# Performance work log

Measured on AMD Instinct MI355X. Metric: run time of the kernel, lower is better.

The kernel has to match this reference:

```python
import jax, jax.numpy as jnp
import numpy as np

HIDDEN = 1024
NUM_HEADS = 16
HEAD_SIZE = HIDDEN // NUM_HEADS


def setup_inputs() -> dict:
    key = jax.random.key(0)
    ks = jax.random.split(key, 5)
    B, S = 2, 2048
    x = jax.random.normal(ks[0], (B, S, HIDDEN), dtype=jnp.float32)
    # nn.Linear(hidden, 3*hidden): weight stored (in, out) for x @ W
    scale_qkv = 1.0 / np.sqrt(HIDDEN)
    w_qkv = jax.random.uniform(ks[1], (HIDDEN, 3 * HIDDEN), minval=-scale_qkv, maxval=scale_qkv, dtype=jnp.float32)
    b_qkv = jax.random.uniform(ks[2], (3 * HIDDEN,), minval=-scale_qkv, maxval=scale_qkv, dtype=jnp.float32)
    w_o = jax.random.uniform(ks[3], (HIDDEN, HIDDEN), minval=-scale_qkv, maxval=scale_qkv, dtype=jnp.float32)
    b_o = jax.random.uniform(ks[4], (HIDDEN,), minval=-scale_qkv, maxval=scale_qkv, dtype=jnp.float32)
    return {"x": x, "w_qkv": w_qkv, "b_qkv": b_qkv, "w_o": w_o, "b_o": b_o}


def reference(x, w_qkv, b_qkv, w_o, b_o):
    B, S, H = x.shape
    qkv = x @ w_qkv + b_qkv  # (B, S, 3H)
    q, k, v = jnp.split(qkv, 3, axis=-1)
    # (B, S, H) -> (B, nheads, S, head_size)
    def heads(t):
        return t.reshape(B, S, NUM_HEADS, HEAD_SIZE).transpose(0, 2, 1, 3)
    q, k, v = heads(q), heads(k), heads(v)
    scores = jnp.einsum('bhqd,bhkd->bhqk', q, k) / np.sqrt(HEAD_SIZE).astype(np.float32)
    causal = jnp.tril(jnp.ones((S, S), dtype=bool))  # k <= q
    scores = jnp.where(causal, scores, -jnp.inf)
    probs = jax.nn.softmax(scores, axis=-1)
    out = jnp.einsum('bhqk,bhkd->bqhd', probs, v).reshape(B, S, H)
    return out @ w_o + b_o
```

## Files before the change

kernel.cpp:

```cpp
#include <hip/hip_runtime.h>
#include <stdint.h>


typedef __bf16 bf16;
typedef __attribute__((ext_vector_type(8))) __bf16 bf16x8;
typedef __attribute__((ext_vector_type(4))) __bf16 bf16x4;
typedef __attribute__((ext_vector_type(4))) float floatx4;
typedef __attribute__((ext_vector_type(16))) float floatx16;

#define SCL 0.18033688011112042f

__device__ __forceinline__ floatx4 mfma_bf16(bf16x8 a, bf16x8 b, floatx4 c) {
  return __builtin_amdgcn_mfma_f32_16x16x32_bf16(a, b, c, 0, 0, 0);
}

__device__ __forceinline__ floatx16 mfma32(bf16x8 a, bf16x8 b, floatx16 c) {
  return __builtin_amdgcn_mfma_f32_32x32x16_bf16(a, b, c, 0, 0, 0);
}

__device__ __forceinline__ void cp_g2l_16(const bf16* g, bf16* l) {
  __builtin_amdgcn_global_load_lds(
      (const __attribute__((address_space(1))) void*)g,
      (__attribute__((address_space(3))) void*)l, 16, 0, 0);
}

__device__ __forceinline__ floatx16 zero16() {
  floatx16 z;
#pragma unroll
  for (int i = 0; i < 16; ++i) z[i] = 0.f;
  return z;
}

__global__ __launch_bounds__(256) void prep_kernel(
    const float* __restrict__ x, bf16* __restrict__ xb,
    const float* __restrict__ w_qkv, bf16* __restrict__ wqkvt,
    const float* __restrict__ w_o, bf16* __restrict__ wot) {
  const int b = blockIdx.x;
  const int tid = threadIdx.x;
  if (b < 4096) {
    const int i = (b * 256 + tid) * 4;
    floatx4 v = *(const floatx4*)(x + i);
    bf16x4 o;
    o[0] = (bf16)v[0]; o[1] = (bf16)v[1]; o[2] = (bf16)v[2]; o[3] = (bf16)v[3];
    *(bf16x4*)(xb + i) = o;
    return;
  }
  __shared__ float tile[32][33];
  const float* W; bf16* Wt; int K, N, n0, k0;
  if (b < 7168) {
    const int bb = b - 4096;
    W = w_qkv; Wt = wqkvt; K = 1024; N = 3072;
    n0 = (bb % 96) * 32; k0 = (bb / 96) * 32;
  } else {
    const int bb = b - 7168;
    W = w_o; Wt = wot; K = 1024; N = 1024;
    n0 = (bb & 31) * 32; k0 = (bb >> 5) * 32;
  }
  const int tx = tid & 31, ty = tid >> 5;
  for (int i = 0; i < 4; ++i)
    tile[ty + 8 * i][tx] = W[(size_t)(k0 + ty + 8 * i) * N + n0 + tx];
  __syncthreads();
  for (int i = 0; i < 4; ++i)
    Wt[(size_t)(n0 + ty + 8 * i) * K + k0 + tx] = (bf16)tile[tx][ty + 8 * i];
}

template <int MODE, int MI>
__global__ __launch_bounds__(256, 3) void gemm_bt_kernel(
    const bf16* __restrict__ A, const bf16* __restrict__ Bt,
    const float* __restrict__ bias, float* __restrict__ outF,
    bf16* __restrict__ qb, bf16* __restrict__ kb, bf16* __restrict__ vtb,
    int N, int K) {
  constexpr int BM = MI * 32;
  __shared__ bf16 As[BM * 32];
  __shared__ bf16 Bs[128 * 32];
  const int tid = threadIdx.x;
  const int w = tid >> 6, lane = tid & 63;
  const int l16 = lane & 15, quad = lane >> 4;
  const int m0 = blockIdx.y * BM, n0 = blockIdx.x * 128;
  const int wm = (w & 1) * (BM / 2), wn = (w >> 1) * 64;

  const int arow = w * (BM / 4) + (lane >> 2);
  const int acol = (lane & 3) * 8;
  const bf16* Ag = A + (size_t)(m0 + arow) * K + acol;
  bf16* Al = As + arow * 32 + acol;
  const int brow = w * 32 + (lane >> 2);
  const bf16* Bg = Bt + (size_t)(n0 + brow) * K + acol;
  bf16* Bl = Bs + brow * 32 + acol;

  floatx4 acc[MI][4];
#pragma unroll
  for (int i = 0; i < MI; ++i)
#pragma unroll
    for (int j = 0; j < 4; ++j) acc[i][j] = (floatx4){0.f, 0.f, 0.f, 0.f};

  for (int k0 = 0; k0 < K; k0 += 32) {
    __syncthreads();
    cp_g2l_16(Ag + k0, Al);
    if (MI == 4) cp_g2l_16(Ag + (size_t)16 * K + k0, Al + 16 * 32);
    cp_g2l_16(Bg + k0, Bl);
    cp_g2l_16(Bg + (size_t)16 * K + k0, Bl + 16 * 32);
    __syncthreads();
    bf16x8 af[MI], bfr[4];
#pragma unroll
    for (int i = 0; i < MI; ++i)
      af[i] = *(const bf16x8*)(&As[(wm + i * 16 + l16) * 32 + quad * 8]);
#pragma unroll
    for (int j = 0; j < 4; ++j)
      bfr[j] = *(const bf16x8*)(&Bs[(wn + j * 16 + l16) * 32 + quad * 8]);
#pragma unroll
    for (int i = 0; i < MI; ++i)
#pragma unroll
      for (int j = 0; j < 4; ++j)
        acc[i][j] = mfma_bf16(af[i], bfr[j], acc[i][j]);
  }

#pragma unroll
  for (int i = 0; i < MI; ++i)
#pragma unroll
    for (int j = 0; j < 4; ++j) {
      const int nn = n0 + wn + j * 16 + l16;
      const float bv = bias[nn];
      const int mbase = m0 + wm + i * 16 + quad * 4;
      if (MODE == 1) {
#pragma unroll
        for (int r = 0; r < 4; ++r)
          outF[(size_t)(mbase + r) * N + nn] = acc[i][j][r] + bv;
      } else {
        const int which = nn >> 10;
        const int rem = nn & 1023;
        const int h = rem >> 6, d = rem & 63;
        const int b = mbase >> 11, s = mbase & 2047;
        const size_t bh = (size_t)(b * 16 + h);
        if (which == 2) {
          bf16x4 pk;
#pragma unroll
          for (int r = 0; r < 4; ++r) pk[r] = (bf16)(acc[i][j][r] + bv);
          *(bf16x4*)(vtb + (bh * 64 + d) * 2048 + s) = pk;
        } else if (which == 0) {
#pragma unroll
          for (int r = 0; r < 4; ++r)
            qb[(bh * 2048 + s + r) * 64 + d] = (bf16)((acc[i][j][r] + bv) * SCL);
        } else {
#pragma unroll
          for (int r = 0; r < 4; ++r)
            kb[(bh * 2048 + s + r) * 64 + d] = (bf16)(acc[i][j][r] + bv);
        }
      }
    }
}

__global__ __launch_bounds__(256, 3) void attn_kernel(
    const bf16* __restrict__ Qb, const bf16* __restrict__ Kb,
    const bf16* __restrict__ Vtb, bf16* __restrict__ attnb) {
  __shared__ bf16 Ks[2][4096];
  __shared__ bf16 Vs[2][4096];
  __shared__ bf16 Ps[4 * 2304];
  const int bid = blockIdx.x;
  const int bh = (bid & 7) * 4 + ((bid >> 3) & 3);
  const int p = bid >> 5;
  const int tid = threadIdx.x;
  const int w = tid >> 6, lane = tid & 63;
  const int l31 = lane & 31, hi = lane >> 5;
  const int b = bh >> 4, h = bh & 15;
  const bool hw = (w < 2);
  const int gB = 31 - p;
  const int q0A = p * 64 + (w & 1) * 32;
  const int q0B = gB * 64 + (w & 1) * 32;
  const int nt = 32 - p;

  const bf16* Qh = Qb + (size_t)bh * 2048 * 64;
  const bf16* Kh = Kb + (size_t)bh * 2048 * 64;
  const bf16* Vh = Vtb + (size_t)bh * 64 * 2048;
  bf16* Pw = Ps + w * 2304;

  const int c0 = tid, c1 = tid + 256;
  const int kof0 = (c0 >> 3) * 64 + ((((c0 & 7) - (c0 >> 3)) & 7) * 8);
  const int kof1 = (c1 >> 3) * 64 + ((((c1 & 7) - (c1 >> 3)) & 7) * 8);
  const int vof0 = (c0 >> 3) * 2048 + ((((c0 & 7) - (c0 >> 3)) & 7) * 8);
  const int vof1 = (c1 >> 3) * 2048 + ((((c1 & 7) - (c1 >> 3)) & 7) * 8);

  int q0 = hw ? q0A : q0B;
  int wdiag = hw ? p : gB;
  bf16x8 qf[4];
  {
    const bf16* Qr = Qh + (size_t)(q0 + l31) * 64 + hi * 8;
#pragma unroll
    for (int kd = 0; kd < 4; ++kd) qf[kd] = *(const bf16x8*)(Qr + kd * 16);
  }
  bf16x8 ones;
#pragma unroll
  for (int j = 0; j < 8; ++j) ones[j] = (bf16)1.0f;

  floatx16 O0 = zero16(), O1 = zero16(), Ol = zero16();

  auto do_ms = [&](int ms, const bf16* KsC, int t, bool diag, int q0c) {
    floatx16 sf = zero16();
    const int row = ms * 32 + l31;
#pragma unroll
    for (int kd = 0; kd < 4; ++kd) {
      bf16x8 kf = *(const bf16x8*)(
          &KsC[row * 64 + (((kd * 2 + hi) + row) & 7) * 8]);
      sf = mfma32(kf, qf[kd], sf);
    }
#pragma unroll
    for (int a = 0; a < 4; ++a) {
      bf16x4 pk;
#pragma unroll
      for (int bq = 0; bq < 4; ++bq) {
        float s = sf[a * 4 + bq];
        if (diag) {
          const int kc = t * 64 + ms * 32 + bq + 8 * a + 4 * hi;
          s = (kc <= q0c + l31) ? s : -1e30f;
        }
        pk[bq] = (bf16)__builtin_amdgcn_exp2f(s);
      }
      *(bf16x4*)(&Pw[l31 * 72 + ms * 32 + 8 * a + 4 * hi]) = pk;
    }
  };

  auto ld_p = [&](int ks) {
    return *(const bf16x8*)(&Pw[l31 * 72 + ks * 16 + hi * 8]);
  };

  auto pv_ks = [&](const bf16* VsC, bf16x8 pfk, int ks) {
    const int r0 = l31, r1 = 32 + l31;
    bf16x8 v0 = *(const bf16x8*)(
        &VsC[r0 * 64 + (((ks * 2 + hi) + r0) & 7) * 8]);
    O0 = mfma32(pfk, v0, O0);
    bf16x8 v1 = *(const bf16x8*)(
        &VsC[r1 * 64 + (((ks * 2 + hi) + r1) & 7) * 8]);
    O1 = mfma32(pfk, v1, O1);
    Ol = mfma32(pfk, ones, Ol);
  };

  auto outW = [&](int qb) {
#pragma unroll
    for (int r = 0; r < 16; ++r) {
      const int q = qb + (r & 3) + 8 * (r >> 2) + 4 * hi;
      const float inv = 1.f / Ol[r];
      bf16* dst = attnb + ((size_t)(b * 2048 + q)) * 1024 + h * 64;
      dst[l31] = (bf16)(O0[r] * inv);
      dst[32 + l31] = (bf16)(O1[r] * inv);
    }
  };

  cp_g2l_16(Kh + kof0, &Ks[0][c0 * 8]);
  cp_g2l_16(Kh + kof1, &Ks[0][c1 * 8]);
  cp_g2l_16(Vh + vof0, &Vs[0][c0 * 8]);
  cp_g2l_16(Vh + vof1, &Vs[0][c1 * 8]);

  int cur = 0;
  for (int t = 0; t < nt; ++t, cur ^= 1) {
    __syncthreads();
    if (t + 1 < nt) {
      const int nb = cur ^ 1;
      cp_g2l_16(Kh + (size_t)(t + 1) * 4096 + kof0, &Ks[nb][c0 * 8]);
      cp_g2l_16(Kh + (size_t)(t + 1) * 4096 + kof1, &Ks[nb][c1 * 8]);
      cp_g2l_16(Vh + (size_t)(t + 1) * 64 + vof0, &Vs[nb][c0 * 8]);
      cp_g2l_16(Vh + (size_t)(t + 1) * 64 + vof1, &Vs[nb][c1 * 8]);
    }
    const bf16* KsC = Ks[cur];
    const bf16* VsC = Vs[cur];
    const bool full = (t <= p);
    const bool diag = (t == wdiag);

    if (full) {
      do_ms(0, KsC, t, diag, q0);
      do_ms(1, KsC, t, diag, q0);
      bf16x8 p0 = ld_p(0), p1 = ld_p(1), p2 = ld_p(2), p3 = ld_p(3);
      pv_ks(VsC, p0, 0); pv_ks(VsC, p1, 1);
      pv_ks(VsC, p2, 2); pv_ks(VsC, p3, 3);
    } else if (hw) {
      do_ms(1, KsC, t, diag, q0);
      bf16x8 p2 = ld_p(2), p3 = ld_p(3);
      pv_ks(VsC, p2, 2); pv_ks(VsC, p3, 3);
    } else {
      do_ms(0, KsC, t, diag, q0);
      bf16x8 p0 = ld_p(0), p1 = ld_p(1);
      pv_ks(VsC, p0, 0); pv_ks(VsC, p1, 1);
    }

    if (hw && t == p) {
      outW(q0A);
      O0 = zero16(); O1 = zero16(); Ol = zero16();
      q0 = q0B; wdiag = gB;
      const bf16* Qr = Qh + (size_t)(q0B + l31) * 64 + hi * 8;
#pragma unroll
      for (int kd = 0; kd < 4; ++kd) qf[kd] = *(const bf16x8*)(Qr + kd * 16);
    }
  }

  __syncthreads();
  float* sO = (float*)(&Vs[0][0]);
  float* sL = (float*)(&Ks[0][0]);
  if (hw) {
#pragma unroll
    for (int r = 0; r < 16; ++r) {
      const int ql = (r & 3) + 8 * (r >> 2) + 4 * hi;
      sO[w * 2048 + ql * 64 + l31] = O0[r];
      sO[w * 2048 + ql * 64 + 32 + l31] = O1[r];
      if (l31 == 0) sL[w * 32 + ql] = Ol[r];
    }
  }
  __syncthreads();
  if (!hw) {
    const int pw = w - 2;
#pragma unroll
    for (int r = 0; r < 16; ++r) {
      const int ql = (r & 3) + 8 * (r >> 2) + 4 * hi;
      O0[r] += sO[pw * 2048 + ql * 64 + l31];
      O1[r] += sO[pw * 2048 + ql * 64 + 32 + l31];
      Ol[r] += sL[pw * 32 + ql];
    }
    outW(q0B);
  }
}

extern "C" void kernel_launch(void* const* d_in, const int* in_sizes, int n_in,
                              void* d_out, int out_size, void* d_ws, size_t ws_size,
                              hipStream_t stream) {
  const float* x     = (const float*)d_in[0];
  const float* w_qkv = (const float*)d_in[1];
  const float* b_qkv = (const float*)d_in[2];
  const float* w_o   = (const float*)d_in[3];
  const float* b_o   = (const float*)d_in[4];
  float* out = (float*)d_out;

  char* ws = (char*)d_ws;
  bf16* xb    = (bf16*)ws; ws += (size_t)4096 * 1024 * 2;
  bf16* wqkvt = (bf16*)ws; ws += (size_t)3072 * 1024 * 2;
  bf16* wot   = (bf16*)ws; ws += (size_t)1024 * 1024 * 2;
  bf16* qb    = (bf16*)ws; ws += (size_t)32 * 2048 * 64 * 2;
  bf16* kb    = (bf16*)ws; ws += (size_t)32 * 2048 * 64 * 2;
  bf16* vtb   = (bf16*)ws; ws += (size_t)32 * 2048 * 64 * 2;
  bf16* attnb = (bf16*)ws; ws += (size_t)4096 * 1024 * 2;

  prep_kernel<<<8192, 256, 0, stream>>>(x, xb, w_qkv, wqkvt, w_o, wot);
  gemm_bt_kernel<0, 4><<<dim3(24, 32), 256, 0, stream>>>(
      xb, wqkvt, b_qkv, nullptr, qb, kb, vtb, 3072, 1024);
  attn_kernel<<<512, 256, 0, stream>>>(qb, kb, vtb, attnb);
  gemm_bt_kernel<1, 2><<<dim3(8, 64), 256, 0, stream>>>(
      attnb, wot, b_o, out, nullptr, nullptr, nullptr, 1024, 1024);
}
```

Baseline: 198.8 us.

## Split attention work per 64-query block and pass P via permlane swaps

Restructures the attention kernel so each block handles a single 64-query tile, with four waves arranged as two query strips times two key halves. The grid doubles and the tiles are ordered for causal load balance. The softmax probabilities are now rearranged into MFMA operand layout in registers with permlane32_swap instead of a round trip through an LDS P buffer. Removing that buffer lowers LDS use, which allows 4 blocks per CU. The cost is a cross-wave reduction in every block and more blocks re-streaming the same K/V.

```diff
diff --git a/kernel.cpp b/kernel.cpp
--- a/kernel.cpp
+++ b/kernel.cpp
@@ -7,6 +7,8 @@
 typedef __attribute__((ext_vector_type(4))) __bf16 bf16x4;
 typedef __attribute__((ext_vector_type(4))) float floatx4;
 typedef __attribute__((ext_vector_type(16))) float floatx16;
+typedef __attribute__((ext_vector_type(4))) unsigned int uint4v;
+typedef __attribute__((ext_vector_type(2))) unsigned int uint2v;
 
 #define SCL 0.18033688011112042f
 
@@ -29,6 +31,23 @@
 #pragma unroll
   for (int i = 0; i < 16; ++i) z[i] = 0.f;
   return z;
+}
+
+__device__ __forceinline__ uint32_t pack2(float lo, float hi2) {
+  union { bf16 h[2]; uint32_t u; } x;
+  x.h[0] = (bf16)lo; x.h[1] = (bf16)hi2;
+  return x.u;
+}
+
+__device__ __forceinline__ uint2v permswap(uint32_t a, uint32_t b) {
+  return __builtin_amdgcn_permlane32_swap(a, b, false, false);
+}
+
+__device__ __forceinline__ bf16x8 mk_pf(uint32_t w0, uint32_t w1, uint32_t w2,
+                                        uint32_t w3) {
+  union { uint4v u; bf16x8 v; } c;
+  c.u = (uint4v){w0, w1, w2, w3};
+  return c.v;
 }
 
 __global__ __launch_bounds__(256) void prep_kernel(
@@ -149,29 +168,28 @@
     }
 }
 
-__global__ __launch_bounds__(256, 3) void attn_kernel(
+__global__ __launch_bounds__(256, 4) void attn_kernel(
     const bf16* __restrict__ Qb, const bf16* __restrict__ Kb,
     const bf16* __restrict__ Vtb, bf16* __restrict__ attnb) {
   __shared__ bf16 Ks[2][4096];
   __shared__ bf16 Vs[2][4096];
-  __shared__ bf16 Ps[4 * 2304];
   const int bid = blockIdx.x;
-  const int bh = (bid & 7) * 4 + ((bid >> 3) & 3);
-  const int p = bid >> 5;
+  const int c = bid & 255, qq = bid >> 8;
+  const int bh = c & 31;
+  const int kk = c >> 5;
+  const int g = (qq == 0) ? kk : (qq == 1) ? 31 - kk
+              : (qq == 2) ? 8 + kk : 23 - kk;
   const int tid = threadIdx.x;
   const int w = tid >> 6, lane = tid & 63;
   const int l31 = lane & 31, hi = lane >> 5;
+  const int strip = w >> 1, ms = w & 1;
+  const int q0s = g * 64 + strip * 32;
   const int b = bh >> 4, h = bh & 15;
-  const bool hw = (w < 2);
-  const int gB = 31 - p;
-  const int q0A = p * 64 + (w & 1) * 32;
-  const int q0B = gB * 64 + (w & 1) * 32;
-  const int nt = 32 - p;
+  const int nt = g + 1;
 
   const bf16* Qh = Qb + (size_t)bh * 2048 * 64;
   const bf16* Kh = Kb + (size_t)bh * 2048 * 64;
   const bf16* Vh = Vtb + (size_t)bh * 64 * 2048;
-  bf16* Pw = Ps + w * 2304;
 
   const int c0 = tid, c1 = tid + 256;
   const int kof0 = (c0 >> 3) * 64 + ((((c0 & 7) - (c0 >> 3)) & 7) * 8);
@@ -179,11 +197,9 @@
   const int vof0 = (c0 >> 3) * 2048 + ((((c0 & 7) - (c0 >> 3)) & 7) * 8);
   const int vof1 = (c1 >> 3) * 2048 + ((((c1 & 7) - (c1 >> 3)) & 7) * 8);
 
-  int q0 = hw ? q0A : q0B;
-  int wdiag = hw ? p : gB;
   bf16x8 qf[4];
   {
-    const bf16* Qr = Qh + (size_t)(q0 + l31) * 64 + hi * 8;
+    const bf16* Qr = Qh + (size_t)(q0s + l31) * 64 + hi * 8;
 #pragma unroll
     for (int kd = 0; kd < 4; ++kd) qf[kd] = *(const bf16x8*)(Qr + kd * 16);
   }
@@ -192,57 +208,6 @@
   for (int j = 0; j < 8; ++j) ones[j] = (bf16)1.0f;
 
   floatx16 O0 = zero16(), O1 = zero16(), Ol = zero16();
-
-  auto do_ms = [&](int ms, const bf16* KsC, int t, bool diag, int q0c) {
-    floatx16 sf = zero16();
-    const int row = ms * 32 + l31;
-#pragma unroll
-    for (int kd = 0; kd < 4; ++kd) {
-      bf16x8 kf = *(const bf16x8*)(
-          &KsC[row * 64 + (((kd * 2 + hi) + row) & 7) * 8]);
-      sf = mfma32(kf, qf[kd], sf);
-    }
-#pragma unroll
-    for (int a = 0; a < 4; ++a) {
-      bf16x4 pk;
-#pragma unroll
-      for (int bq = 0; bq < 4; ++bq) {
-        float s = sf[a * 4 + bq];
-        if (diag) {
-          const int kc = t * 64 + ms * 32 + bq + 8 * a + 4 * hi;
-          s = (kc <= q0c + l31) ? s : -1e30f;
-        }
-        pk[bq] = (bf16)__builtin_amdgcn_exp2f(s);
-      }
-      *(bf16x4*)(&Pw[l31 * 72 + ms * 32 + 8 * a + 4 * hi]) = pk;
-    }
-  };
-
-  auto ld_p = [&](int ks) {
-    return *(const bf16x8*)(&Pw[l31 * 72 + ks * 16 + hi * 8]);
-  };
-
-  auto pv_ks = [&](const bf16* VsC, bf16x8 pfk, int ks) {
-    const int r0 = l31, r1 = 32 + l31;
-    bf16x8 v0 = *(const bf16x8*)(
-        &VsC[r0 * 64 + (((ks * 2 + hi) + r0) & 7) * 8]);
-    O0 = mfma32(pfk, v0, O0);
-    bf16x8 v1 = *(const bf16x8*)(
-        &VsC[r1 * 64 + (((ks * 2 + hi) + r1) & 7) * 8]);
-    O1 = mfma32(pfk, v1, O1);
-    Ol = mfma32(pfk, ones, Ol);
-  };
-
-  auto outW = [&](int qb) {
-#pragma unroll
-    for (int r = 0; r < 16; ++r) {
-      const int q = qb + (r & 3) + 8 * (r >> 2) + 4 * hi;
-      const float inv = 1.f / Ol[r];
-      bf16* dst = attnb + ((size_t)(b * 2048 + q)) * 1024 + h * 64;
-      dst[l31] = (bf16)(O0[r] * inv);
-      dst[32 + l31] = (bf16)(O1[r] * inv);
-    }
-  };
 
   cp_g2l_16(Kh + kof0, &Ks[0][c0 * 8]);
   cp_g2l_16(Kh + kof1, &Ks[0][c1 * 8]);
@@ -259,60 +224,85 @@
       cp_g2l_16(Vh + (size_t)(t + 1) * 64 + vof0, &Vs[nb][c0 * 8]);
       cp_g2l_16(Vh + (size_t)(t + 1) * 64 + vof1, &Vs[nb][c1 * 8]);
     }
+    const bool diag = (t == g);
+    if (diag && strip == 0 && ms == 1) continue;
     const bf16* KsC = Ks[cur];
     const bf16* VsC = Vs[cur];
-    const bool full = (t <= p);
-    const bool diag = (t == wdiag);
-
-    if (full) {
-      do_ms(0, KsC, t, diag, q0);
-      do_ms(1, KsC, t, diag, q0);
-      bf16x8 p0 = ld_p(0), p1 = ld_p(1), p2 = ld_p(2), p3 = ld_p(3);
-      pv_ks(VsC, p0, 0); pv_ks(VsC, p1, 1);
-      pv_ks(VsC, p2, 2); pv_ks(VsC, p3, 3);
-    } else if (hw) {
-      do_ms(1, KsC, t, diag, q0);
-      bf16x8 p2 = ld_p(2), p3 = ld_p(3);
-      pv_ks(VsC, p2, 2); pv_ks(VsC, p3, 3);
-    } else {
-      do_ms(0, KsC, t, diag, q0);
-      bf16x8 p0 = ld_p(0), p1 = ld_p(1);
-      pv_ks(VsC, p0, 0); pv_ks(VsC, p1, 1);
-    }
-
-    if (hw && t == p) {
-      outW(q0A);
-      O0 = zero16(); O1 = zero16(); Ol = zero16();
-      q0 = q0B; wdiag = gB;
-      const bf16* Qr = Qh + (size_t)(q0B + l31) * 64 + hi * 8;
-#pragma unroll
-      for (int kd = 0; kd < 4; ++kd) qf[kd] = *(const bf16x8*)(Qr + kd * 16);
-    }
+
+    floatx16 sf = zero16();
+    const int row = ms * 32 + l31;
+#pragma unroll
+    for (int kd = 0; kd < 4; ++kd) {
+      bf16x8 kf = *(const bf16x8*)(
+          &KsC[row * 64 + (((kd * 2 + hi) + row) & 7) * 8]);
+      sf = mfma32(kf, qf[kd], sf);
+    }
+
+    const int ksA = ms * 2, ksB = ms * 2 + 1;
+    const int r0 = l31, r1 = 32 + l31;
+    bf16x8 va0 = *(const bf16x8*)(&VsC[r0 * 64 + (((ksA * 2 + hi) + r0) & 7) * 8]);
+    bf16x8 va1 = *(const bf16x8*)(&VsC[r1 * 64 + (((ksA * 2 + hi) + r1) & 7) * 8]);
+    bf16x8 vb0 = *(const bf16x8*)(&VsC[r0 * 64 + (((ksB * 2 + hi) + r0) & 7) * 8]);
+    bf16x8 vb1 = *(const bf16x8*)(&VsC[r1 * 64 + (((ksB * 2 + hi) + r1) & 7) * 8]);
+
+    float e[16];
+#pragma unroll
+    for (int r = 0; r < 16; ++r) {
+      float s = sf[r];
+      if (diag) {
+        const int kc = t * 64 + ms * 32 + (r & 3) + 8 * (r >> 2) + 4 * hi;
+        s = (kc <= q0s + l31) ? s : -1e30f;
+      }
+      e[r] = __builtin_amdgcn_exp2f(s);
+    }
+
+    uint32_t W[8];
+#pragma unroll
+    for (int i = 0; i < 8; ++i) W[i] = pack2(e[2 * i], e[2 * i + 1]);
+    uint2v s0 = permswap(W[0], W[2]);
+    uint2v s1 = permswap(W[1], W[3]);
+    bf16x8 pa = mk_pf(s0.x, s1.x, s0.y, s1.y);
+    uint2v s2 = permswap(W[4], W[6]);
+    uint2v s3 = permswap(W[5], W[7]);
+    bf16x8 pb = mk_pf(s2.x, s3.x, s2.y, s3.y);
+
+    O0 = mfma32(pa, va0, O0);
+    O1 = mfma32(pa, va1, O1);
+    Ol = mfma32(pa, ones, Ol);
+    O0 = mfma32(pb, vb0, O0);
+    O1 = mfma32(pb, vb1, O1);
+    Ol = mfma32(pb, ones, Ol);
   }
 
   __syncthreads();
-  float* sO = (float*)(&Vs[0][0]);
-  float* sL = (float*)(&Ks[0][0]);
-  if (hw) {
+  float* fO = (float*)(&Ks[0][0]);
+  float* fL = (float*)(&Vs[0][0]);
+  if (ms == 1) {
 #pragma unroll
     for (int r = 0; r < 16; ++r) {
       const int ql = (r & 3) + 8 * (r >> 2) + 4 * hi;
-      sO[w * 2048 + ql * 64 + l31] = O0[r];
-      sO[w * 2048 + ql * 64 + 32 + l31] = O1[r];
-      if (l31 == 0) sL[w * 32 + ql] = Ol[r];
+      fO[strip * 2048 + ql * 64 + l31] = O0[r];
+      fO[strip * 2048 + ql * 64 + 32 + l31] = O1[r];
+      if (l31 == 0) fL[strip * 32 + ql] = Ol[r];
     }
   }
   __syncthreads();
-  if (!hw) {
-    const int pw = w - 2;
+  if (ms == 0) {
 #pragma unroll
     for (int r = 0; r < 16; ++r) {
       const int ql = (r & 3) + 8 * (r >> 2) + 4 * hi;
-      O0[r] += sO[pw * 2048 + ql * 64 + l31];
-      O1[r] += sO[pw * 2048 + ql * 64 + 32 + l31];
-      Ol[r] += sL[pw * 32 + ql];
-    }
-    outW(q0B);
+      O0[r] += fO[strip * 2048 + ql * 64 + l31];
+      O1[r] += fO[strip * 2048 + ql * 64 + 32 + l31];
+      Ol[r] += fL[strip * 32 + ql];
+    }
+#pragma unroll
+    for (int r = 0; r < 16; ++r) {
+      const int q = q0s + (r & 3) + 8 * (r >> 2) + 4 * hi;
+      const float inv = 1.f / Ol[r];
+      bf16* dst = attnb + ((size_t)(b * 2048 + q)) * 1024 + h * 64;
+      dst[l31] = (bf16)(O0[r] * inv);
+      dst[32 + l31] = (bf16)(O1[r] * inv);
+    }
   }
 }
 
@@ -338,7 +328,7 @@
   prep_kernel<<<8192, 256, 0, stream>>>(x, xb, w_qkv, wqkvt, w_o, wot);
   gemm_bt_kernel<0, 4><<<dim3(24, 32), 256, 0, stream>>>(
       xb, wqkvt, b_qkv, nullptr, qb, kb, vtb, 3072, 1024);
-  attn_kernel<<<512, 256, 0, stream>>>(qb, kb, vtb, attnb);
+  attn_kernel<<<1024, 256, 0, stream>>>(qb, kb, vtb, attnb);
   gemm_bt_kernel<1, 2><<<dim3(8, 64), 256, 0, stream>>>(
       attnb, wot, b_o, out, nullptr, nullptr, nullptr, 1024, 1024);
 }
```

After: 176.4 us. 11.3% less time.
